# Performance work log

Hardware: AMD Instinct MI355X
Metric: run time of the kernel (lower is better)

## Reference

```python
import jax, jax.numpy as jnp
import numpy as np

# Config constants (from CantorExpertConfig)
EXPERT_ID = 2
NUM_EXPERTS = 8
FULL = 4096
EDIM = 1024
SLICE = FULL // NUM_EXPERTS            # 512
OVERLAP = 0.5
_base = 1.0 / NUM_EXPERTS
_ext = _base * OVERLAP
FP_MIN = max(0.0, EXPERT_ID / NUM_EXPERTS - _ext)          # 0.1875
FP_MAX = min(1.0, (EXPERT_ID + 1) / NUM_EXPERTS + _ext)    # 0.4375
SL_START = EXPERT_ID * SLICE
SL_END = SL_START + SLICE
B, P = 4, 4096


def setup_inputs() -> dict:
    key = jax.random.key(0)
    ks = jax.random.split(key, 10)
    tokens = jax.random.normal(ks[0], (B, P, FULL), jnp.float32)
    fingerprints = jax.random.uniform(ks[1], (P,), jnp.float32)
    # gate MLP: Linear(SLICE, SLICE//4) -> GELU -> Linear(SLICE//4, 1) -> Sigmoid
    W_g1 = jax.random.normal(ks[2], (SLICE // 4, SLICE), jnp.float32) / np.sqrt(SLICE)
    b_g1 = jnp.zeros((SLICE // 4,), jnp.float32)
    W_g2 = jax.random.normal(ks[3], (1, SLICE // 4), jnp.float32) / np.sqrt(SLICE // 4)
    b_g2 = jnp.zeros((1,), jnp.float32)
    alpha = jnp.float32(1.0)  # alpha_init
    # xavier-ish init, gain 0.5
    scale = 0.5 * np.sqrt(2.0 / (SLICE + EDIM))
    Wq = jax.random.normal(ks[4], (EDIM, SLICE), jnp.float32) * scale
    Wk = jax.random.normal(ks[5], (EDIM, SLICE), jnp.float32) * scale
    Wv = jax.random.normal(ks[6], (EDIM, SLICE), jnp.float32) * scale
    penta = jax.random.normal(ks[7], (5, EDIM), jnp.float32) * 0.02
    penta = penta / jnp.linalg.norm(penta, axis=-1, keepdims=True)
    return {
        "tokens": tokens, "fingerprints": fingerprints,
        "W_g1": W_g1, "b_g1": b_g1, "W_g2": W_g2, "b_g2": b_g2,
        "alpha": alpha, "Wq": Wq, "Wk": Wk, "Wv": Wv,
        "pentachoron": penta,
    }


def reference(tokens, fingerprints, W_g1, b_g1, W_g2, b_g2, alpha, Wq, Wk, Wv, pentachoron):
    # boolean fingerprint-region mask -> concrete gather indices (eager, outside jit)
    mask = (fingerprints >= FP_MIN) & (fingerprints < FP_MAX)
    idx = jnp.nonzero(mask)[0]                      # [Psel]
    # masked token gather + feature slice: [B, Psel, SLICE]
    my = tokens[:, idx, SL_START:SL_END]
    # gated-MLP alpha gate (torch GELU is exact/erf)
    h = jax.nn.gelu(my @ W_g1.T + b_g1, approximate=False)
    gate = jax.nn.sigmoid(h @ W_g2.T + b_g2)        # [B, Psel, 1]
    aw = jax.nn.sigmoid(alpha)
    my = my * (gate * aw + (1.0 - aw))
    # QKV projections (no bias)
    Q = my @ Wq.T                                   # [B, Psel, EDIM]
    K = my @ Wk.T
    V = my @ Wv.T
    # pentachoron 5-way vertex projections, batched over the 5 vertices
    dirs = pentachoron / jnp.linalg.norm(pentachoron, axis=-1, keepdims=True)  # [5, EDIM]
    Qp = jnp.einsum('bpd,vd->vbp', Q, dirs)         # [5, B, Psel]
    Kp = jnp.einsum('bpd,vd->vbp', K, dirs)
    Vp = jnp.einsum('bpd,vd->vbp', V, dirs)
    return (Q, K, V, Qp, Kp, Vp)
```

## Files before the change

### kernel.cpp

```cpp
#include <hip/hip_runtime.h>
#include <hip/hip_bf16.h>
#include <math.h>

#define PTOK 4096
#define BDIM 4
#define FULLD 4096
#define SLICE 512
#define SL_START 1024
#define EDIM 1024
#define FP_MIN_C 0.1875f
#define FP_MAX_C 0.4375f

typedef __attribute__((ext_vector_type(8))) short bf16x8;
typedef __attribute__((ext_vector_type(4))) float f32x4;

__device__ __forceinline__ unsigned short f2bf(float f) {
    unsigned int u = __float_as_uint(f);
    unsigned int r = (u + 0x7fffu + ((u >> 16) & 1u)) >> 16;
    return (unsigned short)r;
}

__device__ __forceinline__ void gl2lds16(const void* g, void* l) {
    __builtin_amdgcn_global_load_lds(
        (const __attribute__((address_space(1))) unsigned int*)g,
        (__attribute__((address_space(3))) unsigned int*)(unsigned long long)(uintptr_t)l,
        16, 0, 0);
}

__global__ __launch_bounds__(1024) void prep_kernel(const float* __restrict__ fp,
                                                    int* __restrict__ idx,
                                                    const float* __restrict__ penta,
                                                    float* __restrict__ dirs,
                                                    const float* __restrict__ Wq,
                                                    const float* __restrict__ Wk,
                                                    const float* __restrict__ Wv,
                                                    unsigned short* __restrict__ Wb) {
    int blk = blockIdx.x;
    int t = threadIdx.x;
    if (blk == 0) {
        int m[4];
        int c = 0;
#pragma unroll
        for (int i = 0; i < 4; ++i) {
            float f = fp[t * 4 + i];
            m[i] = (f >= FP_MIN_C && f < FP_MAX_C) ? 1 : 0;
            c += m[i];
        }
        int lane = t & 63, wv = t >> 6;
        int inc = c;
#pragma unroll
        for (int off = 1; off < 64; off <<= 1) {
            int n = __shfl_up(inc, off, 64);
            if (lane >= off) inc += n;
        }
        __shared__ int wsum[16];
        if (lane == 63) wsum[wv] = inc;
        __syncthreads();
        if (t < 16) {
            int v = wsum[t];
            int in2 = v;
#pragma unroll
            for (int off = 1; off < 16; off <<= 1) {
                int n = __shfl_up(in2, off, 16);
                if (t >= off) in2 += n;
            }
            wsum[t] = in2 - v;
        }
        __syncthreads();
        int pos = wsum[wv] + inc - c;
#pragma unroll
        for (int i = 0; i < 4; ++i) {
            if (m[i]) idx[pos++] = t * 4 + i;
        }
    } else if (blk <= 5) {
        int v = blk - 1;
        float4 p = make_float4(0.f, 0.f, 0.f, 0.f);
        float ss = 0.f;
        if (t < 256) {
            p = ((const float4*)(penta + (size_t)v * EDIM))[t];
            ss = p.x * p.x + p.y * p.y + p.z * p.z + p.w * p.w;
        }
        for (int off = 32; off > 0; off >>= 1) ss += __shfl_down(ss, off, 64);
        __shared__ float dsum[16];
        if ((t & 63) == 0) dsum[t >> 6] = ss;
        __syncthreads();
        if (t < 256) {
            float tot = dsum[0] + dsum[1] + dsum[2] + dsum[3];
            float inv = 1.0f / sqrtf(tot);
            float4 o = make_float4(p.x * inv, p.y * inv, p.z * inv, p.w * inv);
            ((float4*)(dirs + (size_t)v * EDIM))[t] = o;
        }
    } else {
        int i = (blk - 6) * 1024 + t;
        int mat = i >> 17;
        int rem = i & 131071;
        const float* src = (mat == 0) ? Wq : ((mat == 1) ? Wk : Wv);
        float4 v = ((const float4*)src)[rem];
        ushort4 o;
        o.x = f2bf(v.x); o.y = f2bf(v.y); o.z = f2bf(v.z); o.w = f2bf(v.w);
        ((ushort4*)(Wb + (size_t)mat * EDIM * SLICE))[rem] = o;
    }
}

#define GT 8
__global__ __launch_bounds__(256) void gate_kernel(const float* __restrict__ tokens,
                                                   const int* __restrict__ idx,
                                                   const float* __restrict__ Wg1,
                                                   const float* __restrict__ bg1,
                                                   const float* __restrict__ Wg2,
                                                   const float* __restrict__ bg2,
                                                   const float* __restrict__ alpha,
                                                   unsigned short* __restrict__ Ag,
                                                   int Ntok, int M) {
    __shared__ float rows[GT][SLICE];
    __shared__ float hred[GT][128];
    __shared__ float ssc[GT];

    int tid = threadIdx.x;
    int tok0 = blockIdx.x * GT;

#pragma unroll
    for (int i = 0; i < 4; ++i) {
        int flat = i * 256 + tid;
        int tk = flat >> 7, c4 = flat & 127;
        int g = tok0 + tk;
        if (g >= M) g = M - 1;
        int b = g / Ntok;
        int j = g - b * Ntok;
        int p = idx[j];
        const float4* src = (const float4*)(tokens + ((size_t)b * PTOK + p) * FULLD + SL_START);
        ((float4*)rows[tk])[c4] = src[c4];
    }
    __syncthreads();

    int hidx = tid & 127;
    int grp = tid >> 7;
    const float4* w4 = (const float4*)(Wg1 + (size_t)hidx * SLICE);
    float bias = bg1[hidx];
    float acc[4] = {bias, bias, bias, bias};
#pragma unroll 4
    for (int k = 0; k < SLICE / 4; ++k) {
        float4 w = w4[k];
#pragma unroll
        for (int t8 = 0; t8 < 4; ++t8) {
            float4 r = ((const float4*)rows[grp * 4 + t8])[k];
            acc[t8] += r.x * w.x + r.y * w.y + r.z * w.z + r.w * w.w;
        }
    }
    float wg2 = Wg2[hidx];
#pragma unroll
    for (int t8 = 0; t8 < 4; ++t8) {
        float a = acc[t8];
        float hg = 0.5f * a * (1.0f + erff(a * 0.70710678118654752f));
        hred[grp * 4 + t8][hidx] = hg * wg2;
    }
    __syncthreads();

    int wv = tid >> 6, l = tid & 63;
    float aw = 1.0f / (1.0f + expf(-alpha[0]));
#pragma unroll
    for (int z = 0; z < 2; ++z) {
        int tk = wv * 2 + z;
        float v = hred[tk][l] + hred[tk][l + 64];
        for (int off = 32; off > 0; off >>= 1) v += __shfl_down(v, off, 64);
        if (l == 0) {
            float logit = v + bg2[0];
            float gate = 1.0f / (1.0f + expf(-logit));
            ssc[tk] = gate * aw + (1.0f - aw);
        }
    }
    __syncthreads();

#pragma unroll
    for (int i = 0; i < 4; ++i) {
        int flat = i * 256 + tid;
        int tk = flat >> 7, c4 = flat & 127;
        int g = tok0 + tk;
        if (g < M) {
            float4 r = ((const float4*)rows[tk])[c4];
            float s = ssc[tk];
            ushort4 o;
            o.x = f2bf(r.x * s); o.y = f2bf(r.y * s);
            o.z = f2bf(r.z * s); o.w = f2bf(r.w * s);
            ((ushort4*)(Ag + (size_t)g * SLICE))[c4] = o;
        }
    }
}

__global__ __launch_bounds__(256) void qkv_mfma(const unsigned short* __restrict__ Ag,
                                                const unsigned short* __restrict__ Wb,
                                                float* __restrict__ out, int M) {
    __shared__ short As[2][128 * 32];
    __shared__ short Bs[2][128 * 32];

    const unsigned short* W = Wb + (size_t)blockIdx.z * EDIM * SLICE;
    float* C = out + (size_t)blockIdx.z * M * EDIM;

    int tid = threadIdx.x;
    int bm = blockIdx.y * 128;
    int bn = blockIdx.x * 128;
    int l = tid & 63;
    int w = tid >> 6;
    int wr = w >> 1, wc = w & 1;
    int lane16 = l & 15, kq = l >> 4;

    int srow = tid >> 2;
    int scol = (tid & 3) * 8;

    f32x4 acc[4][4] = {};

    for (int k0 = 0; k0 < SLICE; k0 += 64) {
#pragma unroll
        for (int p = 0; p < 2; ++p) {
#pragma unroll
            for (int r = 0; r < 2; ++r) {
                int arow = bm + r * 64 + srow;
                if (arow >= M) arow = M - 1;
                gl2lds16(Ag + (size_t)arow * SLICE + k0 + p * 32 + scol,
                         &As[p][(r * 64 + srow) * 32 + scol]);
                int brow = bn + r * 64 + srow;
                gl2lds16(W + (size_t)brow * SLICE + k0 + p * 32 + scol,
                         &Bs[p][(r * 64 + srow) * 32 + scol]);
            }
        }
        __syncthreads();

#pragma unroll
        for (int p = 0; p < 2; ++p) {
            bf16x8 a[4], b[4];
#pragma unroll
            for (int i = 0; i < 4; ++i)
                a[i] = *(const bf16x8*)&As[p][(wr * 64 + i * 16 + lane16) * 32 + kq * 8];
#pragma unroll
            for (int j = 0; j < 4; ++j)
                b[j] = *(const bf16x8*)&Bs[p][(wc * 64 + j * 16 + lane16) * 32 + kq * 8];
#pragma unroll
            for (int i = 0; i < 4; ++i)
#pragma unroll
                for (int j = 0; j < 4; ++j)
                    acc[i][j] = __builtin_amdgcn_mfma_f32_16x16x32_bf16(a[i], b[j], acc[i][j], 0, 0, 0);
        }
        __syncthreads();
    }

#pragma unroll
    for (int i = 0; i < 4; ++i) {
        int m0 = bm + wr * 64 + i * 16 + kq * 4;
#pragma unroll
        for (int j = 0; j < 4; ++j) {
            int n = bn + wc * 64 + j * 16 + lane16;
            f32x4 v = acc[i][j];
#pragma unroll
            for (int r = 0; r < 4; ++r) {
                int m = m0 + r;
                if (m < M) C[(size_t)m * EDIM + n] = v[r];
            }
        }
    }
}

__global__ __launch_bounds__(256) void proj_kernel(const float* __restrict__ qkv,
                                                   const float* __restrict__ dirs,
                                                   float* __restrict__ outp, int M) {
    __shared__ float dsh[5 * EDIM];
    int t = threadIdx.x;
#pragma unroll
    for (int i = 0; i < 5; ++i) {
        ((float4*)dsh)[i * 256 + t] = ((const float4*)dirs)[i * 256 + t];
    }
    __syncthreads();

    int gw = blockIdx.x * 4 + (t >> 6);
    if (gw >= 3 * M) return;
    int l = t & 63;
    int q = gw / M;
    int m = gw - q * M;

    const float4* row = (const float4*)(qkv + ((size_t)q * M + m) * EDIM);
    float acc[5] = {0.f, 0.f, 0.f, 0.f, 0.f};
#pragma unroll
    for (int it = 0; it < 4; ++it) {
        int c4 = it * 64 + l;
        float4 v = row[c4];
#pragma unroll
        for (int v5 = 0; v5 < 5; ++v5) {
            float4 d = ((const float4*)dsh)[v5 * 256 + c4];
            acc[v5] += v.x * d.x + v.y * d.y + v.z * d.z + v.w * d.w;
        }
    }
#pragma unroll
    for (int v5 = 0; v5 < 5; ++v5) {
        float a = acc[v5];
        for (int off = 32; off > 0; off >>= 1) a += __shfl_down(a, off, 64);
        if (l == 0) outp[(size_t)(q * 5 + v5) * M + m] = a;
    }
}

extern "C" void kernel_launch(void* const* d_in, const int* in_sizes, int n_in,
                              void* d_out, int out_size, void* d_ws, size_t ws_size,
                              hipStream_t stream) {
    const float* tokens = (const float*)d_in[0];
    const float* fp     = (const float*)d_in[1];
    const float* Wg1    = (const float*)d_in[2];
    const float* bg1    = (const float*)d_in[3];
    const float* Wg2    = (const float*)d_in[4];
    const float* bg2    = (const float*)d_in[5];
    const float* alpha  = (const float*)d_in[6];
    const float* Wq     = (const float*)d_in[7];
    const float* Wk     = (const float*)d_in[8];
    const float* Wv     = (const float*)d_in[9];
    const float* penta  = (const float*)d_in[10];
    float* out = (float*)d_out;

    int Ntok = out_size / 12348;
    int M = BDIM * Ntok;

    char* ws = (char*)d_ws;
    int*            idx  = (int*)ws;
    unsigned short* Ag   = (unsigned short*)(ws + (32 << 10));
    unsigned short* Wb   = (unsigned short*)(ws + (8 << 20));
    float*          dirs = (float*)(ws + (12 << 20));

    prep_kernel<<<390, 1024, 0, stream>>>(fp, idx, penta, dirs, Wq, Wk, Wv, Wb);
    gate_kernel<<<(M + GT - 1) / GT, 256, 0, stream>>>(tokens, idx, Wg1, bg1, Wg2, bg2,
                                                       alpha, Ag, Ntok, M);

    dim3 gg(EDIM / 128, (M + 127) / 128, 3);
    qkv_mfma<<<gg, 256, 0, stream>>>(Ag, Wb, out, M);

    proj_kernel<<<(3 * M + 3) / 4, 256, 0, stream>>>(out, dirs, out + (size_t)3 * M * EDIM, M);
}
```

Measured before the change: 387.3 us.

## Load MFMA operands directly from global and hold projection dirs in registers

The QKV GEMM drops its LDS staging and barriers. Each wave now loads its bf16 A/B fragments straight from global memory into registers, double-buffered across 32-wide K steps. The projection kernel keeps the five direction vectors in registers and has each wave loop over 16 rows, which removes the per-block LDS fill of dirs and cuts the block count. The trade-off is that A/B tiles are no longer shared between waves through LDS, so global/L2 traffic per block roughly doubles, and register pressure rises in both kernels.

Result: slower. 430.8 us (+11.2%).

```diff
diff --git a/kernel.cpp b/kernel.cpp
--- a/kernel.cpp
+++ b/kernel.cpp
@@ -18,13 +18,6 @@
     unsigned int u = __float_as_uint(f);
     unsigned int r = (u + 0x7fffu + ((u >> 16) & 1u)) >> 16;
     return (unsigned short)r;
-}
-
-__device__ __forceinline__ void gl2lds16(const void* g, void* l) {
-    __builtin_amdgcn_global_load_lds(
-        (const __attribute__((address_space(1))) unsigned int*)g,
-        (__attribute__((address_space(3))) unsigned int*)(unsigned long long)(uintptr_t)l,
-        16, 0, 0);
 }
 
 __global__ __launch_bounds__(1024) void prep_kernel(const float* __restrict__ fp,
@@ -190,9 +183,6 @@
 __global__ __launch_bounds__(256) void qkv_mfma(const unsigned short* __restrict__ Ag,
                                                 const unsigned short* __restrict__ Wb,
                                                 float* __restrict__ out, int M) {
-    __shared__ short As[2][128 * 32];
-    __shared__ short Bs[2][128 * 32];
-
     const unsigned short* W = Wb + (size_t)blockIdx.z * EDIM * SLICE;
     float* C = out + (size_t)blockIdx.z * M * EDIM;
 
@@ -204,43 +194,41 @@
     int wr = w >> 1, wc = w & 1;
     int lane16 = l & 15, kq = l >> 4;
 
-    int srow = tid >> 2;
-    int scol = (tid & 3) * 8;
+    const unsigned short* aptr[4];
+    const unsigned short* bptr[4];
+#pragma unroll
+    for (int i = 0; i < 4; ++i) {
+        int m = bm + wr * 64 + i * 16 + lane16;
+        if (m >= M) m = M - 1;
+        aptr[i] = Ag + (size_t)m * SLICE + kq * 8;
+        int n = bn + wc * 64 + i * 16 + lane16;
+        bptr[i] = W + (size_t)n * SLICE + kq * 8;
+    }
 
     f32x4 acc[4][4] = {};
-
-    for (int k0 = 0; k0 < SLICE; k0 += 64) {
-#pragma unroll
-        for (int p = 0; p < 2; ++p) {
-#pragma unroll
-            for (int r = 0; r < 2; ++r) {
-                int arow = bm + r * 64 + srow;
-                if (arow >= M) arow = M - 1;
-                gl2lds16(Ag + (size_t)arow * SLICE + k0 + p * 32 + scol,
-                         &As[p][(r * 64 + srow) * 32 + scol]);
-                int brow = bn + r * 64 + srow;
-                gl2lds16(W + (size_t)brow * SLICE + k0 + p * 32 + scol,
-                         &Bs[p][(r * 64 + srow) * 32 + scol]);
+    bf16x8 a0[4], b0[4], a1[4], b1[4];
+#pragma unroll
+    for (int i = 0; i < 4; ++i) {
+        a0[i] = *(const bf16x8*)(aptr[i]);
+        b0[i] = *(const bf16x8*)(bptr[i]);
+    }
+
+#pragma unroll
+    for (int k0 = 32; k0 <= SLICE; k0 += 32) {
+        if (k0 < SLICE) {
+#pragma unroll
+            for (int i = 0; i < 4; ++i) {
+                a1[i] = *(const bf16x8*)(aptr[i] + k0);
+                b1[i] = *(const bf16x8*)(bptr[i] + k0);
             }
         }
-        __syncthreads();
-
-#pragma unroll
-        for (int p = 0; p < 2; ++p) {
-            bf16x8 a[4], b[4];
-#pragma unroll
-            for (int i = 0; i < 4; ++i)
-                a[i] = *(const bf16x8*)&As[p][(wr * 64 + i * 16 + lane16) * 32 + kq * 8];
+#pragma unroll
+        for (int i = 0; i < 4; ++i)
 #pragma unroll
             for (int j = 0; j < 4; ++j)
-                b[j] = *(const bf16x8*)&Bs[p][(wc * 64 + j * 16 + lane16) * 32 + kq * 8];
-#pragma unroll
-            for (int i = 0; i < 4; ++i)
-#pragma unroll
-                for (int j = 0; j < 4; ++j)
-                    acc[i][j] = __builtin_amdgcn_mfma_f32_16x16x32_bf16(a[i], b[j], acc[i][j], 0, 0, 0);
-        }
-        __syncthreads();
+                acc[i][j] = __builtin_amdgcn_mfma_f32_16x16x32_bf16(a0[i], b0[j], acc[i][j], 0, 0, 0);
+#pragma unroll
+        for (int i = 0; i < 4; ++i) { a0[i] = a1[i]; b0[i] = b1[i]; }
     }
 
 #pragma unroll
@@ -262,37 +250,42 @@
 __global__ __launch_bounds__(256) void proj_kernel(const float* __restrict__ qkv,
                                                    const float* __restrict__ dirs,
                                                    float* __restrict__ outp, int M) {
-    __shared__ float dsh[5 * EDIM];
     int t = threadIdx.x;
-#pragma unroll
-    for (int i = 0; i < 5; ++i) {
-        ((float4*)dsh)[i * 256 + t] = ((const float4*)dirs)[i * 256 + t];
-    }
-    __syncthreads();
-
-    int gw = blockIdx.x * 4 + (t >> 6);
-    if (gw >= 3 * M) return;
     int l = t & 63;
-    int q = gw / M;
-    int m = gw - q * M;
-
-    const float4* row = (const float4*)(qkv + ((size_t)q * M + m) * EDIM);
-    float acc[5] = {0.f, 0.f, 0.f, 0.f, 0.f};
-#pragma unroll
-    for (int it = 0; it < 4; ++it) {
-        int c4 = it * 64 + l;
-        float4 v = row[c4];
+    int wv = t >> 6;
+
+    float4 d[5][4];
+#pragma unroll
+    for (int v5 = 0; v5 < 5; ++v5)
+#pragma unroll
+        for (int it = 0; it < 4; ++it)
+            d[v5][it] = ((const float4*)dirs)[v5 * 256 + it * 64 + l];
+
+    int row0 = (blockIdx.x * 4 + wv) * 16;
+    int total = 3 * M;
+#pragma unroll 1
+    for (int rr = 0; rr < 16; ++rr) {
+        int r = row0 + rr;
+        if (r >= total) return;
+        const float4* row = (const float4*)(qkv + (size_t)r * EDIM);
+        float acc5[5] = {0.f, 0.f, 0.f, 0.f, 0.f};
+#pragma unroll
+        for (int it = 0; it < 4; ++it) {
+            float4 v = row[it * 64 + l];
+#pragma unroll
+            for (int v5 = 0; v5 < 5; ++v5) {
+                acc5[v5] += v.x * d[v5][it].x + v.y * d[v5][it].y +
+                            v.z * d[v5][it].z + v.w * d[v5][it].w;
+            }
+        }
+        int q = r / M;
+        int m = r - q * M;
 #pragma unroll
         for (int v5 = 0; v5 < 5; ++v5) {
-            float4 d = ((const float4*)dsh)[v5 * 256 + c4];
-            acc[v5] += v.x * d.x + v.y * d.y + v.z * d.z + v.w * d.w;
-        }
-    }
-#pragma unroll
-    for (int v5 = 0; v5 < 5; ++v5) {
-        float a = acc[v5];
-        for (int off = 32; off > 0; off >>= 1) a += __shfl_down(a, off, 64);
-        if (l == 0) outp[(size_t)(q * 5 + v5) * M + m] = a;
+            float a = acc5[v5];
+            for (int off = 32; off > 0; off >>= 1) a += __shfl_down(a, off, 64);
+            if (l == 0) outp[(size_t)(q * 5 + v5) * M + m] = a;
+        }
     }
 }
 
@@ -328,5 +321,5 @@
     dim3 gg(EDIM / 128, (M + 127) / 128, 3);
     qkv_mfma<<<gg, 256, 0, stream>>>(Ag, Wb, out, M);
 
-    proj_kernel<<<(3 * M + 3) / 4, 256, 0, stream>>>(out, dirs, out + (size_t)3 * M * EDIM, M);
-}
+    proj_kernel<<<(3 * M + 63) / 64, 256, 0, stream>>>(out, dirs, out + (size_t)3 * M * EDIM, M);
+}
```
